# Kernel tuning notes

Measured on AMD Instinct MI355X. Metric: run time of the kernel, lower is better.

The kernel has to match this reference:

```python
import jax, jax.numpy as jnp
import numpy as np

VOCAB, D, L, H, B, S = 10000, 512, 6, 8, 32, 384
DK = D // H
DFF = 4 * D
EPS = 1e-5


def setup_inputs() -> dict:
    key = jax.random.key(0)
    ks = jax.random.split(key, 24)
    sc = 0.02
    emb = jax.random.normal(ks[0], (VOCAB, D), jnp.float32) * sc
    emb = emb.at[0].set(0.0)  # padding_idx=0
    inp = {
        'input_id': jax.random.randint(ks[1], (B, S), 0, VOCAB),
        'intensity': jax.random.uniform(ks[2], (B, 1, S), jnp.float32),
        'emb': emb,
        'iw': jax.random.normal(ks[3], (1, D), jnp.float32) * sc,
        'ib': jnp.zeros((D,), jnp.float32),
        'Wq': jax.random.normal(ks[4], (L, D, D), jnp.float32) * sc,
        'bq': jnp.zeros((L, D), jnp.float32),
        'Wk': jax.random.normal(ks[5], (L, D, D), jnp.float32) * sc,
        'bk': jnp.zeros((L, D), jnp.float32),
        'Wv': jax.random.normal(ks[6], (L, D, D), jnp.float32) * sc,
        'bv': jnp.zeros((L, D), jnp.float32),
        'Wo': jax.random.normal(ks[7], (L, D, D), jnp.float32) * sc,
        'bo': jnp.zeros((L, D), jnp.float32),
        'ln1w': jnp.ones((L, D), jnp.float32),
        'ln1b': jnp.zeros((L, D), jnp.float32),
        'ln2w': jnp.ones((L, D), jnp.float32),
        'ln2b': jnp.zeros((L, D), jnp.float32),
        'W1': jax.random.normal(ks[8], (L, D, DFF), jnp.float32) * sc,
        'b1': jnp.zeros((L, DFF), jnp.float32),
        'W2': jax.random.normal(ks[9], (L, DFF, D), jnp.float32) * sc,
        'b2': jnp.zeros((L, D), jnp.float32),
    }
    return inp


def _ln(x, w, b):
    m = jnp.mean(x, axis=-1, keepdims=True)
    v = jnp.mean((x - m) ** 2, axis=-1, keepdims=True)
    return (x - m) / jnp.sqrt(v + EPS) * w + b


def _block(x, pad_mask, Wq, bq, Wk, bk, Wv, bv, Wo, bo, ln1w, ln1b, ln2w, ln2b, W1, b1, W2, b2):
    b, s, d = x.shape
    h = _ln(x, ln1w, ln1b)
    q = (h @ Wq + bq).reshape(b, s, H, DK).transpose(0, 2, 1, 3)  # [B,H,S,DK]
    k = (h @ Wk + bk).reshape(b, s, H, DK).transpose(0, 2, 1, 3)
    v = (h @ Wv + bv).reshape(b, s, H, DK).transpose(0, 2, 1, 3)
    scores = jnp.einsum('bhqd,bhkd->bhqk', q, k) / jnp.sqrt(jnp.float32(DK))
    scores = jnp.where(pad_mask, -1e9, scores)  # mask keys at pad positions
    p = jax.nn.softmax(scores, axis=-1)
    attn = jnp.einsum('bhqk,bhkd->bhqd', p, v)
    attn = attn.transpose(0, 2, 1, 3).reshape(b, s, d)
    x = x + (attn @ Wo + bo)
    h2 = _ln(x, ln2w, ln2b)
    ffn = jax.nn.gelu(h2 @ W1 + b1, approximate=False) @ W2 + b2
    return x + ffn


def reference(input_id, intensity, emb, iw, ib, Wq, bq, Wk, bk, Wv, bv, Wo, bo,
              ln1w, ln1b, ln2w, ln2b, W1, b1, W2, b2):
    # predict() path of MSBERT (deterministic; training forward adds random masking)
    inten = jnp.swapaxes(intensity, 1, 2) @ iw + ib          # [B,S,D]
    x = emb[input_id] + inten                                 # token emb + intensity proj
    pad_mask = (input_id == 0)[:, None, None, :]              # [B,1,1,S] broadcast over queries
    for i in range(L):
        x = _block(x, pad_mask, Wq[i], bq[i], Wk[i], bk[i], Wv[i], bv[i], Wo[i], bo[i],
                   ln1w[i], ln1b[i], ln2w[i], ln2b[i], W1[i], b1[i], W2[i], b2[i])
    pool = jnp.matmul(intensity, x) / jnp.float32(intensity.shape[1])  # [B,1,D]
    return pool
```

## Files before the change

kernel.cpp:

```cpp
#include <hip/hip_runtime.h>
#include <math.h>

#define VOCAB 10000
#define D 512
#define L 6
#define H 8
#define B 32
#define S 384
#define DK 64
#define DFF 2048
#define TOK (B * S)
#define TD ((size_t)TOK * D)

typedef unsigned short u16;
using bf16x8 = __attribute__((ext_vector_type(8))) short;
using f32x4  = __attribute__((ext_vector_type(4))) float;
using u16x4  = __attribute__((ext_vector_type(4))) unsigned short;

__device__ u16   g_x[TD];
__device__ u16   g_h[TD];
__device__ u16   g_q[TD];
__device__ u16   g_k[TD];
__device__ u16   g_vt[TD];
__device__ u16   g_ffn[(size_t)TOK * DFF];
__device__ u16   g_qkvT[(size_t)L * 3 * D * D];
__device__ u16   g_woT[(size_t)L * D * D];
__device__ u16   g_w1T[(size_t)L * DFF * D];
__device__ u16   g_w2T[(size_t)L * D * DFF];
__device__ float g_bqkv[L * 3 * D];

__device__ __forceinline__ u16 f2bf(float f) {
  unsigned int u = __builtin_bit_cast(unsigned int, f);
  u = (u + 0x7fffu + ((u >> 16) & 1u)) >> 16;
  return (u16)u;
}
__device__ __forceinline__ float bf2f(u16 v) {
  unsigned int u = ((unsigned int)v) << 16;
  return __builtin_bit_cast(float, u);
}

__device__ __forceinline__ void gld16(const void* g, void* l) {
  __builtin_amdgcn_global_load_lds(
      (const __attribute__((address_space(1))) unsigned int*)g,
      (__attribute__((address_space(3))) unsigned int*)l, 16, 0, 0);
}

__global__ __launch_bounds__(256) void embed_kernel(
    const int* __restrict__ ids, const float* __restrict__ inten,
    const float* __restrict__ emb, const float* __restrict__ iw,
    const float* __restrict__ ib, u16* __restrict__ x) {
  int tok = blockIdx.x;
  int t = threadIdx.x;
  int id = ids[tok];
  float it = inten[tok];
  const float* er = emb + (size_t)id * D;
  u16* xr = x + (size_t)tok * D;
  xr[t]       = f2bf(er[t] + it * iw[t] + ib[t]);
  xr[t + 256] = f2bf(er[t + 256] + it * iw[t + 256] + ib[t + 256]);
}

__global__ __launch_bounds__(256) void ln_kernel(
    const u16* __restrict__ x, const float* __restrict__ w,
    const float* __restrict__ b, u16* __restrict__ out) {
  int tok = blockIdx.x;
  int t = threadIdx.x;
  const u16* xr = x + (size_t)tok * D;
  float v0 = bf2f(xr[t]), v1 = bf2f(xr[t + 256]);
  float s = v0 + v1;
  float ss = v0 * v0 + v1 * v1;
  #pragma unroll
  for (int off = 32; off >= 1; off >>= 1) {
    s += __shfl_down(s, off);
    ss += __shfl_down(ss, off);
  }
  __shared__ float sbuf[4], ssbuf[4];
  int wave = t >> 6, lane = t & 63;
  if (lane == 0) { sbuf[wave] = s; ssbuf[wave] = ss; }
  __syncthreads();
  s = sbuf[0] + sbuf[1] + sbuf[2] + sbuf[3];
  ss = ssbuf[0] + ssbuf[1] + ssbuf[2] + ssbuf[3];
  float mean = s * (1.0f / (float)D);
  float var = ss * (1.0f / (float)D) - mean * mean;
  float rstd = rsqrtf(var + 1e-5f);
  u16* orow = out + (size_t)tok * D;
  orow[t]       = f2bf((v0 - mean) * rstd * w[t] + b[t]);
  orow[t + 256] = f2bf((v1 - mean) * rstd * w[t + 256] + b[t + 256]);
}

__global__ __launch_bounds__(256) void transpose_cvt(
    const float* __restrict__ src, u16* __restrict__ dst,
    int K, int N, size_t sstride, size_t dstride) {
  __shared__ float tile[32][33];
  int n0 = blockIdx.x * 32, k0 = blockIdx.y * 32, l = blockIdx.z;
  src += (size_t)l * sstride;
  dst += (size_t)l * dstride;
  int tx = threadIdx.x & 31, ty = threadIdx.x >> 5;
  #pragma unroll
  for (int i = 0; i < 32; i += 8)
    tile[ty + i][tx] = src[(size_t)(k0 + ty + i) * N + n0 + tx];
  __syncthreads();
  #pragma unroll
  for (int i = 0; i < 32; i += 8)
    dst[(size_t)(n0 + ty + i) * K + k0 + tx] = f2bf(tile[tx][ty + i]);
}

__global__ __launch_bounds__(256) void concat_bias(
    const float* __restrict__ bq, const float* __restrict__ bk,
    const float* __restrict__ bv, float* __restrict__ dst) {
  int i = blockIdx.x * 256 + threadIdx.x;
  int l = i / 1536, c = i % 1536;
  float v = (c < 512) ? bq[l * 512 + c]
          : (c < 1024) ? bk[l * 512 + c - 512]
                       : bv[l * 512 + c - 1024];
  dst[i] = v;
}

template <int EPI>
__global__ __launch_bounds__(256) void mfma_gemm(
    const u16* __restrict__ A, const u16* __restrict__ Bt,
    const float* __restrict__ bias,
    u16* __restrict__ Oq, u16* __restrict__ Ok, u16* __restrict__ Ovt,
    int M, int N, int K) {
  __shared__ u16 As[2][128 * 32];
  __shared__ u16 Bs[2][128 * 32];
  int t = threadIdx.x;
  int lane = t & 63, w = t >> 6;
  int wr = w >> 1, wc = w & 1;

  int gm = gridDim.y, gn = gridDim.x;
  int wgid = blockIdx.y * gn + blockIdx.x;
  int xcd = wgid & 7;
  int c = wgid >> 3;
  int rpx = gm >> 3;
  int cg = c / gn;
  int bm = (xcd * rpx + cg) * 128;
  int bn = (c - cg * gn) * 128;

  int l15 = lane & 15, l4 = lane >> 4;

  int gswu = ((t & 3) ^ ((t >> 3) & 3)) * 8;
  const u16* a0 = A + (size_t)(bm + (t >> 2)) * K + gswu;
  const u16* a1 = A + (size_t)(bm + 64 + (t >> 2)) * K + gswu;
  const u16* b0 = Bt + (size_t)(bn + (t >> 2)) * K + gswu;
  const u16* b1 = Bt + (size_t)(bn + 64 + (t >> 2)) * K + gswu;
  unsigned off0 = (unsigned)(t & 192) * 16u;
  unsigned off1 = off0 + 256u * 16u;
  int rxu = (l4 ^ ((l15 >> 1) & 3)) * 8;

  f32x4 acc[4][4];
  #pragma unroll
  for (int mi = 0; mi < 4; ++mi)
    #pragma unroll
    for (int nj = 0; nj < 4; ++nj)
      acc[mi][nj] = f32x4{0.f, 0.f, 0.f, 0.f};

  int nt = K >> 5;

#define STAGE_T(ti, bi) do { int k0s = (ti) * 32;            \
    gld16(a0 + k0s, (char*)As[bi] + off0);                   \
    gld16(a1 + k0s, (char*)As[bi] + off1);                   \
    gld16(b0 + k0s, (char*)Bs[bi] + off0);                   \
    gld16(b1 + k0s, (char*)Bs[bi] + off1); } while (0)

  STAGE_T(0, 0);
  STAGE_T(1, 1);

  for (int tt = 0; tt < nt; ++tt) {
    if (tt < nt - 1) asm volatile("s_waitcnt vmcnt(4)" ::: "memory");
    else             asm volatile("s_waitcnt vmcnt(0)" ::: "memory");
    __builtin_amdgcn_s_barrier();
    __builtin_amdgcn_sched_barrier(0);
    const u16* Asb = As[tt & 1];
    const u16* Bsb = Bs[tt & 1];
    bf16x8 af[4], bfr[4];
    #pragma unroll
    for (int mi = 0; mi < 4; ++mi)
      af[mi] = *(const bf16x8*)(Asb + (wr * 64 + mi * 16 + l15) * 32 + rxu);
    #pragma unroll
    for (int nj = 0; nj < 4; ++nj)
      bfr[nj] = *(const bf16x8*)(Bsb + (wc * 64 + nj * 16 + l15) * 32 + rxu);
    #pragma unroll
    for (int mi = 0; mi < 4; ++mi)
      #pragma unroll
      for (int nj = 0; nj < 4; ++nj)
        acc[mi][nj] = __builtin_amdgcn_mfma_f32_16x16x32_bf16(af[mi], bfr[nj], acc[mi][nj], 0, 0, 0);
    __builtin_amdgcn_sched_barrier(0);
    __builtin_amdgcn_s_barrier();
    if (tt + 2 < nt) STAGE_T(tt + 2, tt & 1);
  }
#undef STAGE_T

  int row00 = bm + wr * 64, col0 = bn + wc * 64;
  #pragma unroll
  for (int mi = 0; mi < 4; ++mi) {
    int rowb = row00 + mi * 16 + l4 * 4;
    #pragma unroll
    for (int nj = 0; nj < 4; ++nj) {
      int col = col0 + nj * 16 + l15;
      float bcol = bias[col];
      if (EPI == 0) {
        if (col < 512) {
          #pragma unroll
          for (int r = 0; r < 4; ++r)
            Oq[(size_t)(rowb + r) * D + col] = f2bf(acc[mi][nj][r] + bcol);
        } else if (col < 1024) {
          #pragma unroll
          for (int r = 0; r < 4; ++r)
            Ok[(size_t)(rowb + r) * D + (col - 512)] = f2bf(acc[mi][nj][r] + bcol);
        } else {
          int cv = col - 1024;
          int hh = cv >> 6, dk = cv & 63;
          int bb = rowb / S, ss = rowb - bb * S;
          u16x4 pk;
          #pragma unroll
          for (int r = 0; r < 4; ++r) pk[r] = f2bf(acc[mi][nj][r] + bcol);
          *(u16x4*)(Ovt + ((size_t)(bb * H + hh) * DK + dk) * S + ss) = pk;
        }
      } else {
        #pragma unroll
        for (int r = 0; r < 4; ++r) {
          float v = acc[mi][nj][r] + bcol;
          v = 0.5f * v * (1.0f + erff(v * 0.70710678118654752f));
          Oq[(size_t)(rowb + r) * N + col] = f2bf(v);
        }
      }
    }
  }
}

__global__ __launch_bounds__(256) void gemm64(
    const u16* __restrict__ A, const u16* __restrict__ Bt,
    const float* __restrict__ bias, u16* __restrict__ Cres,
    int M, int N, int K) {
  __shared__ u16 As[2][64 * 32];
  __shared__ u16 Bs[2][128 * 32];
  int t = threadIdx.x;
  int lane = t & 63, w = t >> 6;
  int wr = w >> 1, wc = w & 1;

  int gm = gridDim.y, gn = gridDim.x;
  int wgid = blockIdx.y * gn + blockIdx.x;
  int xcd = wgid & 7;
  int c = wgid >> 3;
  int rpx = gm >> 3;
  int cg = c / gn;
  int bm = (xcd * rpx + cg) * 64;
  int bn = (c - cg * gn) * 128;

  int l15 = lane & 15, l4 = lane >> 4;

  int arow = t >> 2, ag = t & 3;
  int aswu = (ag ^ ((arow >> 1) & 3)) * 8;
  const u16* a0 = A + (size_t)(bm + arow) * K + aswu;
  const u16* b0 = Bt + (size_t)(bn + arow) * K + aswu;
  const u16* b1 = Bt + (size_t)(bn + 64 + arow) * K + aswu;
  unsigned offA  = (unsigned)(w * 1024);
  unsigned offB0 = (unsigned)(w * 1024);
  unsigned offB1 = offB0 + 4096u;
  int rxu = (l4 ^ ((l15 >> 1) & 3)) * 8;

  f32x4 acc[2][4];
  #pragma unroll
  for (int mi = 0; mi < 2; ++mi)
    #pragma unroll
    for (int nj = 0; nj < 4; ++nj)
      acc[mi][nj] = f32x4{0.f, 0.f, 0.f, 0.f};

  int nt = K >> 5;

#define STG64(ti, bi) do { int k0s = (ti) * 32;              \
    gld16(a0 + k0s, (char*)As[bi] + offA);                   \
    gld16(b0 + k0s, (char*)Bs[bi] + offB0);                  \
    gld16(b1 + k0s, (char*)Bs[bi] + offB1); } while (0)

  STG64(0, 0);
  STG64(1, 1);

  for (int tt = 0; tt < nt; ++tt) {
    if (tt < nt - 1) asm volatile("s_waitcnt vmcnt(3)" ::: "memory");
    else             asm volatile("s_waitcnt vmcnt(0)" ::: "memory");
    __builtin_amdgcn_s_barrier();
    __builtin_amdgcn_sched_barrier(0);
    const u16* Asb = As[tt & 1];
    const u16* Bsb = Bs[tt & 1];
    bf16x8 af[2], bfr[4];
    #pragma unroll
    for (int mi = 0; mi < 2; ++mi)
      af[mi] = *(const bf16x8*)(Asb + (wr * 32 + mi * 16 + l15) * 32 + rxu);
    #pragma unroll
    for (int nj = 0; nj < 4; ++nj)
      bfr[nj] = *(const bf16x8*)(Bsb + (wc * 64 + nj * 16 + l15) * 32 + rxu);
    #pragma unroll
    for (int mi = 0; mi < 2; ++mi)
      #pragma unroll
      for (int nj = 0; nj < 4; ++nj)
        acc[mi][nj] = __builtin_amdgcn_mfma_f32_16x16x32_bf16(af[mi], bfr[nj], acc[mi][nj], 0, 0, 0);
    __builtin_amdgcn_sched_barrier(0);
    __builtin_amdgcn_s_barrier();
    if (tt + 2 < nt) STG64(tt + 2, tt & 1);
  }
#undef STG64

  int row00 = bm + wr * 32, col0 = bn + wc * 64;
  #pragma unroll
  for (int mi = 0; mi < 2; ++mi) {
    int rowb = row00 + mi * 16 + l4 * 4;
    #pragma unroll
    for (int nj = 0; nj < 4; ++nj) {
      int col = col0 + nj * 16 + l15;
      float bcol = bias[col];
      #pragma unroll
      for (int r = 0; r < 4; ++r) {
        size_t ci = (size_t)(rowb + r) * N + col;
        Cres[ci] = f2bf(bf2f(Cres[ci]) + acc[mi][nj][r] + bcol);
      }
    }
  }
}

__global__ __launch_bounds__(256) void attn_mfma(
    const u16* __restrict__ q, const u16* __restrict__ k,
    const u16* __restrict__ vt, const int* __restrict__ ids,
    u16* __restrict__ out) {
  __shared__ u16 Ks[64][72];
  __shared__ u16 Vs[64][72];
  __shared__ u16 Ps[4][32][72];
  __shared__ float Ms[64];
  int t = threadIdx.x, lane = t & 63, w = t >> 6;
  int l15 = lane & 15, l4 = lane >> 4;
  int bh = blockIdx.x;
  int b = bh >> 3, hh = bh & 7;
  int q0 = blockIdx.y * 128 + w * 32;

  bf16x8 qf[2][2];
  const u16* qbase = q + (size_t)(b * S + q0) * D + hh * DK;
  #pragma unroll
  for (int mi = 0; mi < 2; ++mi)
    #pragma unroll
    for (int ks = 0; ks < 2; ++ks)
      qf[mi][ks] = *(const bf16x8*)(qbase + (size_t)(mi * 16 + l15) * D + ks * 32 + l4 * 8);

  float m[8], lsum[8];
  f32x4 accO[2][4];
  #pragma unroll
  for (int i = 0; i < 8; ++i) { m[i] = -3e38f; lsum[i] = 0.f; }
  #pragma unroll
  for (int mi = 0; mi < 2; ++mi)
    #pragma unroll
    for (int nj = 0; nj < 4; ++nj)
      accO[mi][nj] = f32x4{0.f, 0.f, 0.f, 0.f};

  for (int kb = 0; kb < S; kb += 64) {
    __syncthreads();
    #pragma unroll
    for (int i = 0; i < 2; ++i) {
      int slot = i * 256 + t;
      int rr = slot >> 3, ch = slot & 7;
      *(bf16x8*)(&Ks[rr][ch * 8]) =
          *(const bf16x8*)(k + (size_t)(b * S + kb + rr) * D + hh * DK + ch * 8);
      *(bf16x8*)(&Vs[rr][ch * 8]) =
          *(const bf16x8*)(vt + ((size_t)(b * H + hh) * DK + rr) * S + kb + ch * 8);
    }
    if (t < 64) Ms[t] = (ids[b * S + kb + t] == 0) ? -1e9f : 0.0f;
    __syncthreads();

    f32x4 sc[2][4];
    #pragma unroll
    for (int mi = 0; mi < 2; ++mi)
      #pragma unroll
      for (int nj = 0; nj < 4; ++nj)
        sc[mi][nj] = f32x4{0.f, 0.f, 0.f, 0.f};
    #pragma unroll
    for (int ks = 0; ks < 2; ++ks) {
      bf16x8 kf[4];
      #pragma unroll
      for (int nj = 0; nj < 4; ++nj)
        kf[nj] = *(const bf16x8*)(&Ks[nj * 16 + l15][ks * 32 + l4 * 8]);
      #pragma unroll
      for (int mi = 0; mi < 2; ++mi)
        #pragma unroll
        for (int nj = 0; nj < 4; ++nj)
          sc[mi][nj] = __builtin_amdgcn_mfma_f32_16x16x32_bf16(qf[mi][ks], kf[nj], sc[mi][nj], 0, 0, 0);
    }
    #pragma unroll
    for (int mi = 0; mi < 2; ++mi)
      #pragma unroll
      for (int nj = 0; nj < 4; ++nj) {
        float mv = Ms[nj * 16 + l15];
        #pragma unroll
        for (int r = 0; r < 4; ++r)
          sc[mi][nj][r] = sc[mi][nj][r] * 0.125f + mv;
      }
    #pragma unroll
    for (int mi = 0; mi < 2; ++mi)
      #pragma unroll
      for (int r = 0; r < 4; ++r) {
        int ridx = mi * 4 + r;
        float mx = sc[mi][0][r];
        #pragma unroll
        for (int nj = 1; nj < 4; ++nj) mx = fmaxf(mx, sc[mi][nj][r]);
        #pragma unroll
        for (int o = 1; o < 16; o <<= 1) mx = fmaxf(mx, __shfl_xor(mx, o));
        float mnew = fmaxf(m[ridx], mx);
        float scale = __expf(m[ridx] - mnew);
        float rs = 0.f;
        #pragma unroll
        for (int nj = 0; nj < 4; ++nj) {
          float p = __expf(sc[mi][nj][r] - mnew);
          sc[mi][nj][r] = p;
          rs += p;
        }
        #pragma unroll
        for (int o = 1; o < 16; o <<= 1) rs += __shfl_xor(rs, o);
        lsum[ridx] = lsum[ridx] * scale + rs;
        m[ridx] = mnew;
        #pragma unroll
        for (int nj = 0; nj < 4; ++nj) accO[mi][nj][r] *= scale;
      }
    #pragma unroll
    for (int mi = 0; mi < 2; ++mi)
      #pragma unroll
      for (int nj = 0; nj < 4; ++nj)
        #pragma unroll
        for (int r = 0; r < 4; ++r)
          Ps[w][mi * 16 + l4 * 4 + r][nj * 16 + l15] = f2bf(sc[mi][nj][r]);
    #pragma unroll
    for (int ks2 = 0; ks2 < 2; ++ks2) {
      bf16x8 pf[2], vf[4];
      #pragma unroll
      for (int mi = 0; mi < 2; ++mi)
        pf[mi] = *(const bf16x8*)(&Ps[w][mi * 16 + l15][ks2 * 32 + l4 * 8]);
      #pragma unroll
      for (int nj = 0; nj < 4; ++nj)
        vf[nj] = *(const bf16x8*)(&Vs[nj * 16 + l15][ks2 * 32 + l4 * 8]);
      #pragma unroll
      for (int mi = 0; mi < 2; ++mi)
        #pragma unroll
        for (int nj = 0; nj < 4; ++nj)
          accO[mi][nj] = __builtin_amdgcn_mfma_f32_16x16x32_bf16(pf[mi], vf[nj], accO[mi][nj], 0, 0, 0);
    }
  }

  #pragma unroll
  for (int mi = 0; mi < 2; ++mi)
    #pragma unroll
    for (int nj = 0; nj < 4; ++nj)
      #pragma unroll
      for (int r = 0; r < 4; ++r) {
        int row = b * S + q0 + mi * 16 + l4 * 4 + r;
        out[(size_t)row * D + hh * DK + nj * 16 + l15] =
            f2bf(accO[mi][nj][r] / lsum[mi * 4 + r]);
      }
}

__global__ __launch_bounds__(512) void pool_kernel(
    const u16* __restrict__ x, const float* __restrict__ inten,
    float* __restrict__ out) {
  int b = blockIdx.x;
  int d = threadIdx.x;
  float acc = 0.f;
  for (int s = 0; s < S; ++s)
    acc += inten[b * S + s] * bf2f(x[((size_t)b * S + s) * D + d]);
  out[b * D + d] = acc;
}

extern "C" void kernel_launch(void* const* d_in, const int* in_sizes, int n_in,
                              void* d_out, int out_size, void* d_ws, size_t ws_size,
                              hipStream_t stream) {
  const int* input_id    = (const int*)d_in[0];
  const float* intensity = (const float*)d_in[1];
  const float* emb = (const float*)d_in[2];
  const float* iw  = (const float*)d_in[3];
  const float* ib  = (const float*)d_in[4];
  const float* Wq  = (const float*)d_in[5];
  const float* bq  = (const float*)d_in[6];
  const float* Wk  = (const float*)d_in[7];
  const float* bk  = (const float*)d_in[8];
  const float* Wv  = (const float*)d_in[9];
  const float* bv  = (const float*)d_in[10];
  const float* Wo  = (const float*)d_in[11];
  const float* bo  = (const float*)d_in[12];
  const float* ln1w = (const float*)d_in[13];
  const float* ln1b = (const float*)d_in[14];
  const float* ln2w = (const float*)d_in[15];
  const float* ln2b = (const float*)d_in[16];
  const float* W1  = (const float*)d_in[17];
  const float* b1  = (const float*)d_in[18];
  const float* W2  = (const float*)d_in[19];
  const float* b2  = (const float*)d_in[20];
  float* outp = (float*)d_out;

  float *bqkv;
  u16 *x, *h, *q, *k, *vt, *ffn, *qkvT, *woT, *w1T, *w2T;
  { void* p; hipGetSymbolAddress(&p, HIP_SYMBOL(g_x));    x    = (u16*)p; }
  { void* p; hipGetSymbolAddress(&p, HIP_SYMBOL(g_h));    h    = (u16*)p; }
  { void* p; hipGetSymbolAddress(&p, HIP_SYMBOL(g_q));    q    = (u16*)p; }
  { void* p; hipGetSymbolAddress(&p, HIP_SYMBOL(g_k));    k    = (u16*)p; }
  { void* p; hipGetSymbolAddress(&p, HIP_SYMBOL(g_vt));   vt   = (u16*)p; }
  { void* p; hipGetSymbolAddress(&p, HIP_SYMBOL(g_ffn));  ffn  = (u16*)p; }
  { void* p; hipGetSymbolAddress(&p, HIP_SYMBOL(g_qkvT)); qkvT = (u16*)p; }
  { void* p; hipGetSymbolAddress(&p, HIP_SYMBOL(g_woT));  woT  = (u16*)p; }
  { void* p; hipGetSymbolAddress(&p, HIP_SYMBOL(g_w1T));  w1T  = (u16*)p; }
  { void* p; hipGetSymbolAddress(&p, HIP_SYMBOL(g_w2T));  w2T  = (u16*)p; }
  { void* p; hipGetSymbolAddress(&p, HIP_SYMBOL(g_bqkv)); bqkv = (float*)p; }

  dim3 t256(256);
  transpose_cvt<<<dim3(16, 16, L), t256, 0, stream>>>(Wq, qkvT + 0 * D * D, D, D, (size_t)D * D, (size_t)3 * D * D);
  transpose_cvt<<<dim3(16, 16, L), t256, 0, stream>>>(Wk, qkvT + 1 * D * D, D, D, (size_t)D * D, (size_t)3 * D * D);
  transpose_cvt<<<dim3(16, 16, L), t256, 0, stream>>>(Wv, qkvT + 2 * D * D, D, D, (size_t)D * D, (size_t)3 * D * D);
  transpose_cvt<<<dim3(16, 16, L), t256, 0, stream>>>(Wo, woT, D, D, (size_t)D * D, (size_t)D * D);
  transpose_cvt<<<dim3(64, 16, L), t256, 0, stream>>>(W1, w1T, D, DFF, (size_t)D * DFF, (size_t)D * DFF);
  transpose_cvt<<<dim3(16, 64, L), t256, 0, stream>>>(W2, w2T, DFF, D, (size_t)DFF * D, (size_t)DFF * D);
  concat_bias<<<L * 3 * D / 256, t256, 0, stream>>>(bq, bk, bv, bqkv);

  embed_kernel<<<TOK, t256, 0, stream>>>(input_id, intensity, emb, iw, ib, x);

  for (int l = 0; l < L; ++l) {
    const u16* qkvT_l = qkvT + (size_t)l * 3 * D * D;
    const u16* woT_l  = woT + (size_t)l * D * D;
    const u16* w1T_l  = w1T + (size_t)l * D * DFF;
    const u16* w2T_l  = w2T + (size_t)l * DFF * D;

    ln_kernel<<<TOK, t256, 0, stream>>>(x, ln1w + (size_t)l * D, ln1b + (size_t)l * D, h);
    mfma_gemm<0><<<dim3(12, 96), t256, 0, stream>>>(h, qkvT_l, bqkv + l * 3 * D,
                                                    q, k, vt, TOK, 3 * D, D);
    attn_mfma<<<dim3(B * H, S / 128), t256, 0, stream>>>(q, k, vt, input_id, h);
    gemm64<<<dim3(4, 192), t256, 0, stream>>>(h, woT_l, bo + (size_t)l * D,
                                              x, TOK, D, D);
    ln_kernel<<<TOK, t256, 0, stream>>>(x, ln2w + (size_t)l * D, ln2b + (size_t)l * D, h);
    mfma_gemm<2><<<dim3(16, 96), t256, 0, stream>>>(h, w1T_l, b1 + (size_t)l * DFF,
                                                    ffn, nullptr, nullptr, TOK, DFF, D);
    gemm64<<<dim3(4, 192), t256, 0, stream>>>(ffn, w2T_l, b2 + (size_t)l * D,
                                              x, TOK, D, DFF);
  }

  pool_kernel<<<B, 512, 0, stream>>>(x, intensity, outp);
}
```

Before: 1.314 ms.

## Prefetch K/V in attention, wave-per-row layernorm, split pooling, merge transposes

Attention now computes the pad mask for all keys once and stages the next K/V tile in registers while the current tile computes, with MFMA sections raised in priority; each loop step still has barriers. LayerNorm gives one token per wave with 16-byte vector loads and shuffle-only reductions, removing the LDS reduction and block barrier. Final pooling is split into partial sums over sequence chunks plus a reduce, so more blocks run. The four square weight transposes become one launch. Costs are extra register pressure in attention and an extra launch for pooling.

```diff
diff --git a/kernel.cpp b/kernel.cpp
--- a/kernel.cpp
+++ b/kernel.cpp
@@ -28,6 +28,7 @@
 __device__ u16   g_w1T[(size_t)L * DFF * D];
 __device__ u16   g_w2T[(size_t)L * D * DFF];
 __device__ float g_bqkv[L * 3 * D];
+__device__ float g_pool[B * 6 * D];
 
 __device__ __forceinline__ u16 f2bf(float f) {
   unsigned int u = __builtin_bit_cast(unsigned int, f);
@@ -62,29 +63,37 @@
 __global__ __launch_bounds__(256) void ln_kernel(
     const u16* __restrict__ x, const float* __restrict__ w,
     const float* __restrict__ b, u16* __restrict__ out) {
-  int tok = blockIdx.x;
-  int t = threadIdx.x;
-  const u16* xr = x + (size_t)tok * D;
-  float v0 = bf2f(xr[t]), v1 = bf2f(xr[t + 256]);
-  float s = v0 + v1;
-  float ss = v0 * v0 + v1 * v1;
-  #pragma unroll
-  for (int off = 32; off >= 1; off >>= 1) {
-    s += __shfl_down(s, off);
-    ss += __shfl_down(ss, off);
-  }
-  __shared__ float sbuf[4], ssbuf[4];
-  int wave = t >> 6, lane = t & 63;
-  if (lane == 0) { sbuf[wave] = s; ssbuf[wave] = ss; }
-  __syncthreads();
-  s = sbuf[0] + sbuf[1] + sbuf[2] + sbuf[3];
-  ss = ssbuf[0] + ssbuf[1] + ssbuf[2] + ssbuf[3];
+  int tok = blockIdx.x * 4 + (threadIdx.x >> 6);
+  int lane = threadIdx.x & 63;
+  const u16* xr = x + (size_t)tok * D + lane * 8;
+  bf16x8 v8 = *(const bf16x8*)xr;
+  float v[8];
+  float s = 0.f, ss = 0.f;
+  #pragma unroll
+  for (int i = 0; i < 8; ++i) {
+    v[i] = bf2f((u16)v8[i]);
+    s += v[i];
+    ss += v[i] * v[i];
+  }
+  #pragma unroll
+  for (int o = 1; o < 64; o <<= 1) {
+    s += __shfl_xor(s, o);
+    ss += __shfl_xor(ss, o);
+  }
   float mean = s * (1.0f / (float)D);
   float var = ss * (1.0f / (float)D) - mean * mean;
   float rstd = rsqrtf(var + 1e-5f);
-  u16* orow = out + (size_t)tok * D;
-  orow[t]       = f2bf((v0 - mean) * rstd * w[t] + b[t]);
-  orow[t + 256] = f2bf((v1 - mean) * rstd * w[t + 256] + b[t + 256]);
+  float4 w0 = *(const float4*)(w + lane * 8);
+  float4 w1 = *(const float4*)(w + lane * 8 + 4);
+  float4 b0 = *(const float4*)(b + lane * 8);
+  float4 b1 = *(const float4*)(b + lane * 8 + 4);
+  float wv[8] = {w0.x, w0.y, w0.z, w0.w, w1.x, w1.y, w1.z, w1.w};
+  float bv[8] = {b0.x, b0.y, b0.z, b0.w, b1.x, b1.y, b1.z, b1.w};
+  bf16x8 o8;
+  #pragma unroll
+  for (int i = 0; i < 8; ++i)
+    o8[i] = (short)f2bf((v[i] - mean) * rstd * wv[i] + bv[i]);
+  *(bf16x8*)(out + (size_t)tok * D + lane * 8) = o8;
 }
 
 __global__ __launch_bounds__(256) void transpose_cvt(
@@ -102,6 +111,28 @@
   #pragma unroll
   for (int i = 0; i < 32; i += 8)
     dst[(size_t)(n0 + ty + i) * K + k0 + tx] = f2bf(tile[tx][ty + i]);
+}
+
+__global__ __launch_bounds__(256) void transpose_qkvo(
+    const float* __restrict__ Wq, const float* __restrict__ Wk,
+    const float* __restrict__ Wv, const float* __restrict__ Wo,
+    u16* __restrict__ qkvT, u16* __restrict__ woT) {
+  __shared__ float tile[32][33];
+  int z = blockIdx.z;
+  int l = z >> 2, which = z & 3;
+  const float* src = (which == 0 ? Wq : which == 1 ? Wk : which == 2 ? Wv : Wo)
+                     + (size_t)l * D * D;
+  u16* dst = (which < 3) ? (qkvT + (size_t)l * 3 * D * D + (size_t)which * D * D)
+                         : (woT + (size_t)l * D * D);
+  int n0 = blockIdx.x * 32, k0 = blockIdx.y * 32;
+  int tx = threadIdx.x & 31, ty = threadIdx.x >> 5;
+  #pragma unroll
+  for (int i = 0; i < 32; i += 8)
+    tile[ty + i][tx] = src[(size_t)(k0 + ty + i) * D + n0 + tx];
+  __syncthreads();
+  #pragma unroll
+  for (int i = 0; i < 32; i += 8)
+    dst[(size_t)(n0 + ty + i) * D + k0 + tx] = f2bf(tile[tx][ty + i]);
 }
 
 __global__ __launch_bounds__(256) void concat_bias(
@@ -325,13 +356,16 @@
   __shared__ u16 Ks[64][72];
   __shared__ u16 Vs[64][72];
   __shared__ u16 Ps[4][32][72];
-  __shared__ float Ms[64];
+  __shared__ float Msall[S];
   int t = threadIdx.x, lane = t & 63, w = t >> 6;
   int l15 = lane & 15, l4 = lane >> 4;
   int bh = blockIdx.x;
   int b = bh >> 3, hh = bh & 7;
   int q0 = blockIdx.y * 128 + w * 32;
 
+  for (int i = t; i < S; i += 256)
+    Msall[i] = (ids[b * S + i] == 0) ? -1e9f : 0.0f;
+
   bf16x8 qf[2][2];
   const u16* qbase = q + (size_t)(b * S + q0) * D + hh * DK;
   #pragma unroll
@@ -340,6 +374,22 @@
     for (int ks = 0; ks < 2; ++ks)
       qf[mi][ks] = *(const bf16x8*)(qbase + (size_t)(mi * 16 + l15) * D + ks * 32 + l4 * 8);
 
+  int rr0 = t >> 3, ch0 = t & 7;
+  int rr1 = (256 + t) >> 3, ch1 = t & 7;
+  const size_t kbase = (size_t)(b * S) * D + hh * DK;
+  const size_t vbase = (size_t)(b * H + hh) * DK * S;
+
+  bf16x8 kr0, kr1, vr0, vr1;
+  kr0 = *(const bf16x8*)(k + kbase + (size_t)rr0 * D + ch0 * 8);
+  kr1 = *(const bf16x8*)(k + kbase + (size_t)rr1 * D + ch1 * 8);
+  vr0 = *(const bf16x8*)(vt + vbase + (size_t)rr0 * S + 0 + ch0 * 8);
+  vr1 = *(const bf16x8*)(vt + vbase + (size_t)rr1 * S + 0 + ch1 * 8);
+  *(bf16x8*)(&Ks[rr0][ch0 * 8]) = kr0;
+  *(bf16x8*)(&Ks[rr1][ch1 * 8]) = kr1;
+  *(bf16x8*)(&Vs[rr0][ch0 * 8]) = vr0;
+  *(bf16x8*)(&Vs[rr1][ch1 * 8]) = vr1;
+  __syncthreads();
+
   float m[8], lsum[8];
   f32x4 accO[2][4];
   #pragma unroll
@@ -351,18 +401,13 @@
       accO[mi][nj] = f32x4{0.f, 0.f, 0.f, 0.f};
 
   for (int kb = 0; kb < S; kb += 64) {
-    __syncthreads();
-    #pragma unroll
-    for (int i = 0; i < 2; ++i) {
-      int slot = i * 256 + t;
-      int rr = slot >> 3, ch = slot & 7;
-      *(bf16x8*)(&Ks[rr][ch * 8]) =
-          *(const bf16x8*)(k + (size_t)(b * S + kb + rr) * D + hh * DK + ch * 8);
-      *(bf16x8*)(&Vs[rr][ch * 8]) =
-          *(const bf16x8*)(vt + ((size_t)(b * H + hh) * DK + rr) * S + kb + ch * 8);
+    bool more = (kb + 64) < S;
+    if (more) {
+      kr0 = *(const bf16x8*)(k + kbase + (size_t)(kb + 64 + rr0) * D + ch0 * 8);
+      kr1 = *(const bf16x8*)(k + kbase + (size_t)(kb + 64 + rr1) * D + ch1 * 8);
+      vr0 = *(const bf16x8*)(vt + vbase + (size_t)rr0 * S + kb + 64 + ch0 * 8);
+      vr1 = *(const bf16x8*)(vt + vbase + (size_t)rr1 * S + kb + 64 + ch1 * 8);
     }
-    if (t < 64) Ms[t] = (ids[b * S + kb + t] == 0) ? -1e9f : 0.0f;
-    __syncthreads();
 
     f32x4 sc[2][4];
     #pragma unroll
@@ -370,6 +415,7 @@
       #pragma unroll
       for (int nj = 0; nj < 4; ++nj)
         sc[mi][nj] = f32x4{0.f, 0.f, 0.f, 0.f};
+    __builtin_amdgcn_s_setprio(1);
     #pragma unroll
     for (int ks = 0; ks < 2; ++ks) {
       bf16x8 kf[4];
@@ -382,11 +428,12 @@
         for (int nj = 0; nj < 4; ++nj)
           sc[mi][nj] = __builtin_amdgcn_mfma_f32_16x16x32_bf16(qf[mi][ks], kf[nj], sc[mi][nj], 0, 0, 0);
     }
+    __builtin_amdgcn_s_setprio(0);
     #pragma unroll
     for (int mi = 0; mi < 2; ++mi)
       #pragma unroll
       for (int nj = 0; nj < 4; ++nj) {
-        float mv = Ms[nj * 16 + l15];
+        float mv = Msall[kb + nj * 16 + l15];
         #pragma unroll
         for (int r = 0; r < 4; ++r)
           sc[mi][nj][r] = sc[mi][nj][r] * 0.125f + mv;
@@ -424,6 +471,7 @@
         #pragma unroll
         for (int r = 0; r < 4; ++r)
           Ps[w][mi * 16 + l4 * 4 + r][nj * 16 + l15] = f2bf(sc[mi][nj][r]);
+    __builtin_amdgcn_s_setprio(1);
     #pragma unroll
     for (int ks2 = 0; ks2 < 2; ++ks2) {
       bf16x8 pf[2], vf[4];
@@ -438,6 +486,16 @@
         #pragma unroll
         for (int nj = 0; nj < 4; ++nj)
           accO[mi][nj] = __builtin_amdgcn_mfma_f32_16x16x32_bf16(pf[mi], vf[nj], accO[mi][nj], 0, 0, 0);
+    }
+    __builtin_amdgcn_s_setprio(0);
+
+    if (more) {
+      __syncthreads();
+      *(bf16x8*)(&Ks[rr0][ch0 * 8]) = kr0;
+      *(bf16x8*)(&Ks[rr1][ch1 * 8]) = kr1;
+      *(bf16x8*)(&Vs[rr0][ch0 * 8]) = vr0;
+      *(bf16x8*)(&Vs[rr1][ch1 * 8]) = vr1;
+      __syncthreads();
     }
   }
 
@@ -453,14 +511,23 @@
       }
 }
 
-__global__ __launch_bounds__(512) void pool_kernel(
+__global__ __launch_bounds__(512) void pool_part(
     const u16* __restrict__ x, const float* __restrict__ inten,
-    float* __restrict__ out) {
-  int b = blockIdx.x;
+    float* __restrict__ part) {
+  int b = blockIdx.x, cchunk = blockIdx.y;
   int d = threadIdx.x;
+  int s0 = cchunk * 64;
   float acc = 0.f;
-  for (int s = 0; s < S; ++s)
+  for (int s = s0; s < s0 + 64; ++s)
     acc += inten[b * S + s] * bf2f(x[((size_t)b * S + s) * D + d]);
+  part[((size_t)b * 6 + cchunk) * D + d] = acc;
+}
+__global__ __launch_bounds__(512) void pool_reduce(
+    const float* __restrict__ part, float* __restrict__ out) {
+  int b = blockIdx.x, d = threadIdx.x;
+  float acc = 0.f;
+  #pragma unroll
+  for (int c = 0; c < 6; ++c) acc += part[((size_t)b * 6 + c) * D + d];
   out[b * D + d] = acc;
 }
 
@@ -490,7 +557,7 @@
   const float* b2  = (const float*)d_in[20];
   float* outp = (float*)d_out;
 
-  float *bqkv;
+  float *bqkv, *poolp;
   u16 *x, *h, *q, *k, *vt, *ffn, *qkvT, *woT, *w1T, *w2T;
   { void* p; hipGetSymbolAddress(&p, HIP_SYMBOL(g_x));    x    = (u16*)p; }
   { void* p; hipGetSymbolAddress(&p, HIP_SYMBOL(g_h));    h    = (u16*)p; }
@@ -503,12 +570,10 @@
   { void* p; hipGetSymbolAddress(&p, HIP_SYMBOL(g_w1T));  w1T  = (u16*)p; }
   { void* p; hipGetSymbolAddress(&p, HIP_SYMBOL(g_w2T));  w2T  = (u16*)p; }
   { void* p; hipGetSymbolAddress(&p, HIP_SYMBOL(g_bqkv)); bqkv = (float*)p; }
+  { void* p; hipGetSymbolAddress(&p, HIP_SYMBOL(g_pool)); poolp = (float*)p; }
 
   dim3 t256(256);
-  transpose_cvt<<<dim3(16, 16, L), t256, 0, stream>>>(Wq, qkvT + 0 * D * D, D, D, (size_t)D * D, (size_t)3 * D * D);
-  transpose_cvt<<<dim3(16, 16, L), t256, 0, stream>>>(Wk, qkvT + 1 * D * D, D, D, (size_t)D * D, (size_t)3 * D * D);
-  transpose_cvt<<<dim3(16, 16, L), t256, 0, stream>>>(Wv, qkvT + 2 * D * D, D, D, (size_t)D * D, (size_t)3 * D * D);
-  transpose_cvt<<<dim3(16, 16, L), t256, 0, stream>>>(Wo, woT, D, D, (size_t)D * D, (size_t)D * D);
+  transpose_qkvo<<<dim3(16, 16, 4 * L), t256, 0, stream>>>(Wq, Wk, Wv, Wo, qkvT, woT);
   transpose_cvt<<<dim3(64, 16, L), t256, 0, stream>>>(W1, w1T, D, DFF, (size_t)D * DFF, (size_t)D * DFF);
   transpose_cvt<<<dim3(16, 64, L), t256, 0, stream>>>(W2, w2T, DFF, D, (size_t)DFF * D, (size_t)DFF * D);
   concat_bias<<<L * 3 * D / 256, t256, 0, stream>>>(bq, bk, bv, bqkv);
@@ -521,18 +586,19 @@
     const u16* w1T_l  = w1T + (size_t)l * D * DFF;
     const u16* w2T_l  = w2T + (size_t)l * DFF * D;
 
-    ln_kernel<<<TOK, t256, 0, stream>>>(x, ln1w + (size_t)l * D, ln1b + (size_t)l * D, h);
+    ln_kernel<<<TOK / 4, t256, 0, stream>>>(x, ln1w + (size_t)l * D, ln1b + (size_t)l * D, h);
     mfma_gemm<0><<<dim3(12, 96), t256, 0, stream>>>(h, qkvT_l, bqkv + l * 3 * D,
                                                     q, k, vt, TOK, 3 * D, D);
     attn_mfma<<<dim3(B * H, S / 128), t256, 0, stream>>>(q, k, vt, input_id, h);
     gemm64<<<dim3(4, 192), t256, 0, stream>>>(h, woT_l, bo + (size_t)l * D,
                                               x, TOK, D, D);
-    ln_kernel<<<TOK, t256, 0, stream>>>(x, ln2w + (size_t)l * D, ln2b + (size_t)l * D, h);
+    ln_kernel<<<TOK / 4, t256, 0, stream>>>(x, ln2w + (size_t)l * D, ln2b + (size_t)l * D, h);
     mfma_gemm<2><<<dim3(16, 96), t256, 0, stream>>>(h, w1T_l, b1 + (size_t)l * DFF,
                                                     ffn, nullptr, nullptr, TOK, DFF, D);
     gemm64<<<dim3(4, 192), t256, 0, stream>>>(ffn, w2T_l, b2 + (size_t)l * D,
                                               x, TOK, D, DFF);
   }
 
-  pool_kernel<<<B, 512, 0, stream>>>(x, intensity, outp);
-}
+  pool_part<<<dim3(B, 6), dim3(512), 0, stream>>>(x, intensity, poolp);
+  pool_reduce<<<B, dim3(512), 0, stream>>>(poolp, outp);
+}
```

Result: faster. 1.240 ms, median of 2 (-5.7%).
